# Optimization experiments

Measured on AMD Instinct MI355X. Metric: run time of the kernel, lower is better.

## Reference

```python
import jax, jax.numpy as jnp
import numpy as np

N = 100000   # n_nodes
E = 500000   # n_edges
EH = 256     # e_hidden
RH = 128     # r_hidden
R = 1000     # n_relations (rel.max()+1, pinned in setup)


def _seg_softmax(logits, seg, num_segments):
    # numerically-stable softmax grouped by segment id
    m = jax.ops.segment_max(logits, seg, num_segments=num_segments)
    ex = jnp.exp(logits - m[seg])
    s = jax.ops.segment_sum(ex, seg, num_segments=num_segments)
    return ex / s[seg]


def setup_inputs() -> dict:
    key = jax.random.key(0)
    ks = jax.random.split(key, 14)
    s_e = 1.0 / np.sqrt(EH)
    s_r = 1.0 / np.sqrt(RH)
    x_e = jax.random.normal(ks[0], (N, EH), dtype=jnp.float32)
    edge_index = jax.random.randint(ks[1], (2, E), 0, N, dtype=jnp.int32)
    rel = jax.random.randint(ks[2], (E,), 0, R, dtype=jnp.int32).at[0].set(R - 1)
    rel_all = jax.random.randint(ks[3], (E,), 0, R, dtype=jnp.int32)
    return {
        "x_e": x_e,
        "edge_index": edge_index,
        "rel": rel,
        "rel_all": rel_all,
        "w_h": jax.random.normal(ks[4], (EH, RH), dtype=jnp.float32) * s_e,
        "w_t": jax.random.normal(ks[5], (EH, RH), dtype=jnp.float32) * s_e,
        "a_h1": jax.random.normal(ks[6], (RH,), dtype=jnp.float32) * s_r,
        "a_h2": jax.random.normal(ks[7], (RH,), dtype=jnp.float32) * s_r,
        "a_t1": jax.random.normal(ks[8], (RH,), dtype=jnp.float32) * s_r,
        "a_t2": jax.random.normal(ks[9], (RH,), dtype=jnp.float32) * s_r,
        "r_h_w": jax.random.normal(ks[10], (RH, RH), dtype=jnp.float32) * s_r,
        "r_h_b": jax.random.normal(ks[11], (RH,), dtype=jnp.float32) * s_r,
        "r_t_w": jax.random.normal(ks[12], (RH, RH), dtype=jnp.float32) * s_r,
        "r_t_b": jax.random.normal(ks[13], (RH,), dtype=jnp.float32) * s_r,
    }


def reference(x_e, edge_index, rel, rel_all, w_h, w_t, a_h1, a_h2, a_t1, a_t2,
              r_h_w, r_h_b, r_t_w, r_t_b):
    h_idx, t_idx = edge_index[0], edge_index[1]
    x_r_h = x_e @ w_h          # [N, RH]
    x_r_t = x_e @ w_t          # [N, RH]
    # per-node attention scalars, gathered per edge
    e1 = (x_r_h @ a_h1)[h_idx] + (x_r_t @ a_h2)[t_idx]   # [E]
    e2 = (x_r_h @ a_t1)[h_idx] + (x_r_t @ a_t2)[t_idx]   # [E]
    alpha_h = _seg_softmax(jax.nn.leaky_relu(e1, 0.01), rel, R)
    alpha_t = _seg_softmax(jax.nn.leaky_relu(e2, 0.01), rel, R)
    # sparse.mm(adj, M) == segment-sum over edges of alpha[e] * M[node[e]] into row rel[e]
    msg_h = x_r_h @ r_h_w + r_h_b + x_r_h                 # [N, RH]
    msg_t = x_r_t @ r_t_w + r_t_b + x_r_t                 # [N, RH]
    out_h = jax.ops.segment_sum(alpha_h[:, None] * msg_h[h_idx], rel, num_segments=R)
    out_t = jax.ops.segment_sum(alpha_t[:, None] * msg_t[t_idx], rel, num_segments=R)
    return out_h + out_t                                   # [R, RH]
```

## Files before the change

### kernel.cpp

```cpp
#include <hip/hip_runtime.h>
#include <hip/hip_bf16.h>
#include <math.h>


#define EHD 256
#define RHD 128
#define RMAX 1024
#define HBLK 128
#define SCHUNK 2048
#define SEGMAX 4096

typedef __attribute__((ext_vector_type(8))) short short8;
typedef __attribute__((ext_vector_type(4))) float f32x4;

__device__ __forceinline__ short f2bf(float x) {
    __hip_bfloat16 b = __float2bfloat16(x);
    return *reinterpret_cast<short*>(&b);
}
__device__ __forceinline__ float bfu(unsigned int u) {
    return __uint_as_float(u << 16);
}
__device__ __forceinline__ float leaky(float x) { return x > 0.f ? x : 0.01f * x; }
__device__ __forceinline__ int xswz(int row, int col) {
    return col ^ ((row & 7) << 3);
}

__global__ __launch_bounds__(256) void k_prep2(const float* __restrict__ wh,
                                               const float* __restrict__ wt,
                                               short* __restrict__ whT,
                                               short* __restrict__ wtT)
{
    const float* src = blockIdx.z ? wt : wh;
    short* dst = blockIdx.z ? wtT : whT;
    __shared__ float t[32][33];
    const int k0 = blockIdx.x * 32, n0 = blockIdx.y * 32;
    const int tr = threadIdx.x >> 3, tc = (threadIdx.x & 7) << 2;
    float4 v = *reinterpret_cast<const float4*>(src + (size_t)(k0 + tr) * RHD + n0 + tc);
    t[tr][tc + 0] = v.x; t[tr][tc + 1] = v.y;
    t[tr][tc + 2] = v.z; t[tr][tc + 3] = v.w;
    __syncthreads();
    short* o = dst + (size_t)(n0 + tr) * EHD + k0 + tc;
    o[0] = f2bf(t[tc + 0][tr]); o[1] = f2bf(t[tc + 1][tr]);
    o[2] = f2bf(t[tc + 2][tr]); o[3] = f2bf(t[tc + 3][tr]);
}

__global__ __launch_bounds__(256, 4) void k_fused(
    const float* __restrict__ xe,
    const short* __restrict__ whT, const short* __restrict__ wtT,
    const float* __restrict__ ah1, const float* __restrict__ ah2,
    const float* __restrict__ at1, const float* __restrict__ at2,
    float2* __restrict__ sA, float2* __restrict__ sB,
    short* __restrict__ xrh, short* __restrict__ xrt, int N,
    const int* __restrict__ rel, int* __restrict__ counts, int R, int E)
{
    __shared__ __align__(16) union {
        short Bs[2][2][128][32];
        short Xs[2][64][128];
        int   Hs[RMAX];
    } u;

    const int tid = threadIdx.x;
    const int w = tid >> 6, l = tid & 63;
    const int ln = l & 15, lk = l >> 4;
    const int m0 = blockIdx.x * 64;
    const int orow = (w << 4) + (lk << 2);

    f32x4 acch[8], acct[8];
#pragma unroll
    for (int c = 0; c < 8; c++) {
        acch[c] = (f32x4){0.f, 0.f, 0.f, 0.f};
        acct[c] = (f32x4){0.f, 0.f, 0.f, 0.f};
    }

    const int arow = m0 + (w << 4) + ln;
    const int aclamp = min(arow, N - 1);
    const float* abase = xe + (size_t)aclamp * EHD + (lk << 3);
    short* BsFlat = &u.Bs[0][0][0][0];

    const int Rl = l >> 2, kc = l & 3;

    auto stage = [&](int buf, int kt) {
#pragma unroll
        for (int i = 0; i < 4; i++) {
            const int j = (w << 2) + i;
            const int Rr = (j << 4) + Rl;
            const int mat = Rr >> 7, row = Rr & 127;
            const short* g = (mat ? wtT : whT) + (size_t)row * EHD + kt + (kc << 3);
            __builtin_amdgcn_global_load_lds(
                (const __attribute__((address_space(1))) void*)g,
                (__attribute__((address_space(3))) void*)(BsFlat + (buf << 13) + (j << 9)),
                16, 0, 0);
        }
    };

    float4 a0 = *reinterpret_cast<const float4*>(abase);
    float4 a1 = *reinterpret_cast<const float4*>(abase + 4);
    stage(0, 0);

#pragma unroll
    for (int s = 0; s < 8; s++) {
        const int kt = s << 5;
        __syncthreads();
        if (s < 7) stage((s + 1) & 1, kt + 32);
        short8 af;
        af[0] = f2bf(a0.x); af[1] = f2bf(a0.y); af[2] = f2bf(a0.z); af[3] = f2bf(a0.w);
        af[4] = f2bf(a1.x); af[5] = f2bf(a1.y); af[6] = f2bf(a1.z); af[7] = f2bf(a1.w);
        if (s < 7) {
            a0 = *reinterpret_cast<const float4*>(abase + kt + 32);
            a1 = *reinterpret_cast<const float4*>(abase + kt + 36);
        }
        const int b = s & 1;
#pragma unroll
        for (int c = 0; c < 8; c++) {
            short8 bh = *reinterpret_cast<const short8*>(&u.Bs[b][0][(c << 4) + ln][lk << 3]);
            short8 bt = *reinterpret_cast<const short8*>(&u.Bs[b][1][(c << 4) + ln][lk << 3]);
            acch[c] = __builtin_amdgcn_mfma_f32_16x16x32_bf16(af, bh, acch[c], 0, 0, 0);
            acct[c] = __builtin_amdgcn_mfma_f32_16x16x32_bf16(af, bt, acct[c], 0, 0, 0);
        }
    }
    __syncthreads();

    float p1[4] = {0,0,0,0}, p2[4] = {0,0,0,0}, p3[4] = {0,0,0,0}, p4[4] = {0,0,0,0};
#pragma unroll
    for (int c = 0; c < 8; c++) {
        const int col = (c << 4) + ln;
        const float wa1 = ah1[col], wa2 = ah2[col], wa3 = at1[col], wa4 = at2[col];
#pragma unroll
        for (int r = 0; r < 4; r++) {
            const float vh = acch[c][r], vt = acct[c][r];
            p1[r] = fmaf(vh, wa1, p1[r]);
            p3[r] = fmaf(vh, wa3, p3[r]);
            p2[r] = fmaf(vt, wa2, p2[r]);
            p4[r] = fmaf(vt, wa4, p4[r]);
            const int row = orow + r;
            const int cs = xswz(row, col);
            u.Xs[0][row][cs] = f2bf(vh);
            u.Xs[1][row][cs] = f2bf(vt);
        }
    }
#pragma unroll
    for (int off = 1; off < 16; off <<= 1) {
#pragma unroll
        for (int r = 0; r < 4; r++) {
            p1[r] += __shfl_xor(p1[r], off);
            p2[r] += __shfl_xor(p2[r], off);
            p3[r] += __shfl_xor(p3[r], off);
            p4[r] += __shfl_xor(p4[r], off);
        }
    }
    if (ln == 0) {
#pragma unroll
        for (int r = 0; r < 4; r++) {
            const int grow = m0 + orow + r;
            if (grow < N) {
                sA[grow] = make_float2(p1[r], p3[r]);
                sB[grow] = make_float2(p2[r], p4[r]);
            }
        }
    }
    __syncthreads();
#pragma unroll
    for (int it = 0; it < 8; it++) {
        const int idx = tid + (it << 8);
        const int mat = idx >> 10;
        const int rem = idx & 1023;
        const int row = rem >> 4;
        const int ch  = rem & 15;
        const int grow = m0 + row;
        if (grow < N) {
            const int cs = (ch << 3) ^ ((row & 7) << 3);
            short8 v = *reinterpret_cast<const short8*>(&u.Xs[mat][row][cs]);
            short* dst = (mat ? xrt : xrh) + (size_t)grow * RHD + (ch << 3);
            *reinterpret_cast<short8*>(dst) = v;
        }
    }

    if (blockIdx.x < HBLK) {
        __syncthreads();
        for (int i = tid; i < R; i += 256) u.Hs[i] = 0;
        __syncthreads();
        for (int e = blockIdx.x * 256 + tid; e < E; e += HBLK * 256)
            atomicAdd(&u.Hs[rel[e]], 1);
        __syncthreads();
        for (int i = tid; i < R; i += 256) {
            int v = u.Hs[i];
            if (v) atomicAdd(&counts[i], v);
        }
    }
}

__global__ __launch_bounds__(1024) void k_scan(
    const int* __restrict__ counts, int* __restrict__ starts,
    int* __restrict__ cursor, int R, int E)
{
    __shared__ int buf[2][1024];
    int t = threadIdx.x;
    int v = (t < R) ? counts[t] : 0;
    buf[0][t] = v;
    int cur = 0;
    for (int off = 1; off < 1024; off <<= 1) {
        __syncthreads();
        int x = buf[cur][t];
        if (t >= off) x += buf[cur][t - off];
        buf[cur ^ 1][t] = x;
        cur ^= 1;
    }
    __syncthreads();
    int incl = buf[cur][t];
    if (t < R) { starts[t] = incl - v; cursor[t] = incl - v; }
    if (t == 0) starts[R] = E;
}

__global__ __launch_bounds__(256) void k_scatter(
    const int* __restrict__ rel, int* __restrict__ cursor,
    const int* __restrict__ eh, const int* __restrict__ et,
    const float2* __restrict__ sA, const float2* __restrict__ sB,
    int2* __restrict__ rec1, int2* __restrict__ rec2, int R, int E)
{
    __shared__ int lcnt[RMAX];
    __shared__ int lbase[RMAX];
    const int tid = threadIdx.x;
    const int base = blockIdx.x * SCHUNK;
    const int nE = min(SCHUNK, E - base);
    for (int i = tid; i < R; i += 256) lcnt[i] = 0;
    __syncthreads();
    for (int i = tid; i < nE; i += 256) atomicAdd(&lcnt[rel[base + i]], 1);
    __syncthreads();
    for (int r = tid; r < R; r += 256) {
        int c = lcnt[r];
        lbase[r] = c ? atomicAdd(&cursor[r], c) : 0;
        lcnt[r] = 0;
    }
    __syncthreads();
    for (int i = tid; i < nE; i += 256) {
        const int e = base + i;
        const int r = rel[e];
        const int off = atomicAdd(&lcnt[r], 1);
        const int pos = lbase[r] + off;
        const int h = eh[e], t = et[e];
        const float2 va = sA[h];
        const float2 vb = sB[t];
        const float x1 = __expf(leaky(va.x + vb.x));
        const float x2 = __expf(leaky(va.y + vb.y));
        rec1[pos] = make_int2(h, __float_as_int(x1));
        rec2[pos] = make_int2(t, __float_as_int(x2));
    }
}

__global__ __launch_bounds__(512) void k_rel(
    const int* __restrict__ starts,
    const int2* __restrict__ rec1, const int2* __restrict__ rec2,
    const short* __restrict__ xrh, const short* __restrict__ xrt,
    float* __restrict__ y, int R)
{
    const int r = blockIdx.x;
    const int side = blockIdx.y;
    const int start = starts[r], end = starts[r + 1];
    const int len = end - start;
    if (len <= 0) return;
    const int tid = threadIdx.x;
    const int2* __restrict__ rc = (side ? rec2 : rec1) + start;
    const unsigned short* __restrict__ mb =
        reinterpret_cast<const unsigned short*>(side ? xrt : xrh);

    __shared__ float red[8];
    __shared__ int   lnode[SEGMAX];
    __shared__ float lal[SEGMAX];
    __shared__ float part[8][128];

    const int slot = tid >> 6;
    const int jj = tid & 63;
    float a0 = 0.f, a1 = 0.f;

    if (len <= SEGMAX) {
        float sum = 0.f;
        for (int i = tid; i < len; i += 512) {
            int2 v = rc[i];
            lnode[i] = v.x;
            float x = __int_as_float(v.y);
            lal[i] = x;
            sum += x;
        }
#pragma unroll
        for (int off = 32; off > 0; off >>= 1) sum += __shfl_xor(sum, off);
        if ((tid & 63) == 0) red[slot] = sum;
        __syncthreads();
        sum = ((red[0] + red[1]) + (red[2] + red[3]))
            + ((red[4] + red[5]) + (red[6] + red[7]));
        const float inv = 1.f / sum;

        int q = slot;
        for (; q + 24 < len; q += 32) {
            const float w0 = lal[q] * inv;       const int n0 = lnode[q];
            const float w1 = lal[q + 8] * inv;   const int n1 = lnode[q + 8];
            const float w2 = lal[q + 16] * inv;  const int n2 = lnode[q + 16];
            const float w3 = lal[q + 24] * inv;  const int n3 = lnode[q + 24];
            const unsigned int v0 =
                *reinterpret_cast<const unsigned int*>(mb + (size_t)n0 * RHD + (jj << 1));
            const unsigned int v1 =
                *reinterpret_cast<const unsigned int*>(mb + (size_t)n1 * RHD + (jj << 1));
            const unsigned int v2 =
                *reinterpret_cast<const unsigned int*>(mb + (size_t)n2 * RHD + (jj << 1));
            const unsigned int v3 =
                *reinterpret_cast<const unsigned int*>(mb + (size_t)n3 * RHD + (jj << 1));
            a0 = fmaf(w0, bfu(v0 & 0xffffu), a0);
            a1 = fmaf(w0, bfu(v0 >> 16), a1);
            a0 = fmaf(w1, bfu(v1 & 0xffffu), a0);
            a1 = fmaf(w1, bfu(v1 >> 16), a1);
            a0 = fmaf(w2, bfu(v2 & 0xffffu), a0);
            a1 = fmaf(w2, bfu(v2 >> 16), a1);
            a0 = fmaf(w3, bfu(v3 & 0xffffu), a0);
            a1 = fmaf(w3, bfu(v3 >> 16), a1);
        }
        for (; q < len; q += 8) {
            const float w0 = lal[q] * inv;
            const int   n0 = lnode[q];
            const unsigned int v0 =
                *reinterpret_cast<const unsigned int*>(mb + (size_t)n0 * RHD + (jj << 1));
            a0 = fmaf(w0, bfu(v0 & 0xffffu), a0);
            a1 = fmaf(w0, bfu(v0 >> 16), a1);
        }
    } else {
        float sum = 0.f;
        for (int i = tid; i < len; i += 512) sum += __int_as_float(rc[i].y);
#pragma unroll
        for (int off = 32; off > 0; off >>= 1) sum += __shfl_xor(sum, off);
        if ((tid & 63) == 0) red[slot] = sum;
        __syncthreads();
        sum = ((red[0] + red[1]) + (red[2] + red[3]))
            + ((red[4] + red[5]) + (red[6] + red[7]));
        const float inv = 1.f / sum;

        for (int c0 = 0; c0 < len; c0 += 512) {
            __syncthreads();
            int i = c0 + tid;
            if (i < len) {
                int2 v = rc[i];
                lal[tid] = __int_as_float(v.y) * inv;
                lnode[tid] = v.x;
            }
            __syncthreads();
            const int nc = min(512, len - c0);
            for (int q = slot; q < nc; q += 8) {
                const float wq = lal[q];
                const int n = lnode[q];
                const unsigned int v =
                    *reinterpret_cast<const unsigned int*>(mb + (size_t)n * RHD + (jj << 1));
                a0 = fmaf(wq, bfu(v & 0xffffu), a0);
                a1 = fmaf(wq, bfu(v >> 16), a1);
            }
        }
    }

    part[slot][(jj << 1) + 0] = a0;
    part[slot][(jj << 1) + 1] = a1;
    __syncthreads();
    if (tid < 128) {
        float v = ((part[0][tid] + part[1][tid]) + (part[2][tid] + part[3][tid]))
                + ((part[4][tid] + part[5][tid]) + (part[6][tid] + part[7][tid]));
        y[((size_t)side * R + r) * RHD + tid] = v;
    }
}

__global__ __launch_bounds__(128) void k_out(
    const float* __restrict__ y,
    const float* __restrict__ rhw, const float* __restrict__ rtw,
    const float* __restrict__ rhb, const float* __restrict__ rtb,
    const int* __restrict__ starts,
    float* __restrict__ out, int R)
{
    const int r = blockIdx.x;
    const int j = threadIdx.x;
    __shared__ float ph[RHD], pt[RHD];
    ph[j] = y[(size_t)r * RHD + j];
    pt[j] = y[((size_t)R + r) * RHD + j];
    __syncthreads();
    float acc = ph[j] + pt[j];
    if (starts[r + 1] > starts[r]) acc += rhb[j] + rtb[j];
    float a = 0.f;
#pragma unroll 8
    for (int k = 0; k < RHD; k++) {
        a = fmaf(ph[k], rhw[k * RHD + j], a);
        a = fmaf(pt[k], rtw[k * RHD + j], a);
    }
    out[(size_t)r * RHD + j] = acc + a;
}

extern "C" void kernel_launch(void* const* d_in, const int* in_sizes, int n_in,
                              void* d_out, int out_size, void* d_ws, size_t ws_size,
                              hipStream_t stream)
{
    const float* xe  = (const float*)d_in[0];
    const int*  eidx = (const int*)d_in[1];
    const int*  rel  = (const int*)d_in[2];
    const float* wh  = (const float*)d_in[4];
    const float* wt  = (const float*)d_in[5];
    const float* ah1 = (const float*)d_in[6];
    const float* ah2 = (const float*)d_in[7];
    const float* at1 = (const float*)d_in[8];
    const float* at2 = (const float*)d_in[9];
    const float* rhw = (const float*)d_in[10];
    const float* rhb = (const float*)d_in[11];
    const float* rtw = (const float*)d_in[12];
    const float* rtb = (const float*)d_in[13];
    float* out = (float*)d_out;

    const int N = in_sizes[0] / EHD;
    const int E = in_sizes[2];
    const int R = out_size / RHD;
    const int* eh = eidx;
    const int* et = eidx + E;

    char* ws = (char*)d_ws;
    size_t off = 0;
    auto alloc = [&](size_t bytes) -> void* {
        void* p = ws + off;
        off = (off + bytes + 255) & ~(size_t)255;
        return p;
    };
    short* xrh   = (short*)alloc((size_t)N * RHD * sizeof(short));
    short* xrt   = (short*)alloc((size_t)N * RHD * sizeof(short));
    short* whT   = (short*)alloc((size_t)RHD * EHD * sizeof(short));
    short* wtT   = (short*)alloc((size_t)RHD * EHD * sizeof(short));
    float* y     = (float*)alloc((size_t)2 * R * RHD * sizeof(float));
    float2* sA   = (float2*)alloc((size_t)N * sizeof(float2));
    float2* sB   = (float2*)alloc((size_t)N * sizeof(float2));
    int* counts  = (int*)alloc((size_t)R * sizeof(int));
    int* starts  = (int*)alloc((size_t)(R + 1) * sizeof(int));
    int* cursor  = (int*)alloc((size_t)R * sizeof(int));
    int2* rec1   = (int2*)alloc((size_t)E * sizeof(int2));
    int2* rec2   = (int2*)alloc((size_t)E * sizeof(int2));
    (void)ws_size; (void)n_in;

    hipMemsetAsync(counts, 0, (size_t)R * sizeof(int), stream);
    hipMemsetAsync(y, 0, (size_t)2 * R * RHD * sizeof(float), stream);

    k_prep2<<<dim3(EHD / 32, RHD / 32, 2), 256, 0, stream>>>(wh, wt, whT, wtT);

    k_fused<<<(N + 63) / 64, 256, 0, stream>>>(
        xe, whT, wtT, ah1, ah2, at1, at2,
        sA, sB, xrh, xrt, N, rel, counts, R, E);

    k_scan<<<1, 1024, 0, stream>>>(counts, starts, cursor, R, E);
    k_scatter<<<(E + SCHUNK - 1) / SCHUNK, 256, 0, stream>>>(
        rel, cursor, eh, et, sA, sB, rec1, rec2, R, E);
    k_rel<<<dim3(R, 2), 512, 0, stream>>>(starts, rec1, rec2, xrh, xrt, y, R);
    k_out<<<R, 128, 0, stream>>>(y, rhw, rtw, rhb, rtb, starts, out, R);
}
```

Measured before the change: 122.4 us.

## Fold prefix scan into fused kernel via last-block pattern; merge edge records

Removes the separate single-block scan kernel launch by having the last block of the fused GEMM kernel, detected with a completion counter and thread fences, compute the exclusive prefix over relation counts. It also merges the two per-edge int2 record arrays into one int4 array, so the scatter issues a single 16-byte store per edge. The cost is an extra memset and an atomic per block. k_rel now reads 16 bytes per edge where it needs only 8, which doubles its record traffic.

```diff
diff --git a/kernel.cpp b/kernel.cpp
--- a/kernel.cpp
+++ b/kernel.cpp
@@ -51,13 +51,17 @@
     const float* __restrict__ at1, const float* __restrict__ at2,
     float2* __restrict__ sA, float2* __restrict__ sB,
     short* __restrict__ xrh, short* __restrict__ xrt, int N,
-    const int* __restrict__ rel, int* __restrict__ counts, int R, int E)
+    const int* __restrict__ rel, int* __restrict__ counts,
+    int* __restrict__ starts, int* __restrict__ cursor,
+    int* __restrict__ donecnt, int R, int E)
 {
     __shared__ __align__(16) union {
         short Bs[2][2][128][32];
         short Xs[2][64][128];
         int   Hs[RMAX];
+        int   Sc[2][RMAX];
     } u;
+    __shared__ int lastflag;
 
     const int tid = threadIdx.x;
     const int w = tid >> 6, l = tid & 63;
@@ -187,35 +191,43 @@
             if (v) atomicAdd(&counts[i], v);
         }
     }
-}
-
-__global__ __launch_bounds__(1024) void k_scan(
-    const int* __restrict__ counts, int* __restrict__ starts,
-    int* __restrict__ cursor, int R, int E)
-{
-    __shared__ int buf[2][1024];
-    int t = threadIdx.x;
-    int v = (t < R) ? counts[t] : 0;
-    buf[0][t] = v;
-    int cur = 0;
-    for (int off = 1; off < 1024; off <<= 1) {
-        __syncthreads();
-        int x = buf[cur][t];
-        if (t >= off) x += buf[cur][t - off];
-        buf[cur ^ 1][t] = x;
-        cur ^= 1;
-    }
-    __syncthreads();
-    int incl = buf[cur][t];
-    if (t < R) { starts[t] = incl - v; cursor[t] = incl - v; }
-    if (t == 0) starts[R] = E;
+
+    __threadfence();
+    if (tid == 0) {
+        int prev = atomicAdd(donecnt, 1);
+        lastflag = (prev == (int)gridDim.x - 1);
+    }
+    __syncthreads();
+    if (lastflag) {
+        __threadfence();
+        __syncthreads();
+        for (int i = tid; i < RMAX; i += 256)
+            u.Sc[0][i] = (i < R) ? counts[i] : 0;
+        __syncthreads();
+        int cur = 0;
+        for (int off = 1; off < RMAX; off <<= 1) {
+            for (int i = tid; i < RMAX; i += 256) {
+                int x = u.Sc[cur][i];
+                if (i >= off) x += u.Sc[cur][i - off];
+                u.Sc[cur ^ 1][i] = x;
+            }
+            __syncthreads();
+            cur ^= 1;
+        }
+        for (int i = tid; i < R; i += 256) {
+            const int st = u.Sc[cur][i] - counts[i];
+            starts[i] = st;
+            cursor[i] = st;
+        }
+        if (tid == 0) starts[R] = E;
+    }
 }
 
 __global__ __launch_bounds__(256) void k_scatter(
     const int* __restrict__ rel, int* __restrict__ cursor,
     const int* __restrict__ eh, const int* __restrict__ et,
     const float2* __restrict__ sA, const float2* __restrict__ sB,
-    int2* __restrict__ rec1, int2* __restrict__ rec2, int R, int E)
+    int4* __restrict__ rec, int R, int E)
 {
     __shared__ int lcnt[RMAX];
     __shared__ int lbase[RMAX];
@@ -242,14 +254,13 @@
         const float2 vb = sB[t];
         const float x1 = __expf(leaky(va.x + vb.x));
         const float x2 = __expf(leaky(va.y + vb.y));
-        rec1[pos] = make_int2(h, __float_as_int(x1));
-        rec2[pos] = make_int2(t, __float_as_int(x2));
+        rec[pos] = make_int4(h, __float_as_int(x1), t, __float_as_int(x2));
     }
 }
 
 __global__ __launch_bounds__(512) void k_rel(
     const int* __restrict__ starts,
-    const int2* __restrict__ rec1, const int2* __restrict__ rec2,
+    const int4* __restrict__ rec,
     const short* __restrict__ xrh, const short* __restrict__ xrt,
     float* __restrict__ y, int R)
 {
@@ -259,7 +270,7 @@
     const int len = end - start;
     if (len <= 0) return;
     const int tid = threadIdx.x;
-    const int2* __restrict__ rc = (side ? rec2 : rec1) + start;
+    const int4* __restrict__ rc = rec + start;
     const unsigned short* __restrict__ mb =
         reinterpret_cast<const unsigned short*>(side ? xrt : xrh);
 
@@ -275,9 +286,10 @@
     if (len <= SEGMAX) {
         float sum = 0.f;
         for (int i = tid; i < len; i += 512) {
-            int2 v = rc[i];
-            lnode[i] = v.x;
-            float x = __int_as_float(v.y);
+            int4 v = rc[i];
+            const int node = side ? v.z : v.x;
+            const float x = __int_as_float(side ? v.w : v.y);
+            lnode[i] = node;
             lal[i] = x;
             sum += x;
         }
@@ -322,7 +334,8 @@
         }
     } else {
         float sum = 0.f;
-        for (int i = tid; i < len; i += 512) sum += __int_as_float(rc[i].y);
+        for (int i = tid; i < len; i += 512)
+            sum += __int_as_float(side ? rc[i].w : rc[i].y);
 #pragma unroll
         for (int off = 32; off > 0; off >>= 1) sum += __shfl_xor(sum, off);
         if ((tid & 63) == 0) red[slot] = sum;
@@ -335,9 +348,9 @@
             __syncthreads();
             int i = c0 + tid;
             if (i < len) {
-                int2 v = rc[i];
-                lal[tid] = __int_as_float(v.y) * inv;
-                lnode[tid] = v.x;
+                int4 v = rc[i];
+                lnode[tid] = side ? v.z : v.x;
+                lal[tid] = __int_as_float(side ? v.w : v.y) * inv;
             }
             __syncthreads();
             const int nc = min(512, len - c0);
@@ -428,22 +441,22 @@
     int* counts  = (int*)alloc((size_t)R * sizeof(int));
     int* starts  = (int*)alloc((size_t)(R + 1) * sizeof(int));
     int* cursor  = (int*)alloc((size_t)R * sizeof(int));
-    int2* rec1   = (int2*)alloc((size_t)E * sizeof(int2));
-    int2* rec2   = (int2*)alloc((size_t)E * sizeof(int2));
+    int* donecnt = (int*)alloc(sizeof(int));
+    int4* rec    = (int4*)alloc((size_t)E * sizeof(int4));
     (void)ws_size; (void)n_in;
 
     hipMemsetAsync(counts, 0, (size_t)R * sizeof(int), stream);
+    hipMemsetAsync(donecnt, 0, sizeof(int), stream);
     hipMemsetAsync(y, 0, (size_t)2 * R * RHD * sizeof(float), stream);
 
     k_prep2<<<dim3(EHD / 32, RHD / 32, 2), 256, 0, stream>>>(wh, wt, whT, wtT);
 
     k_fused<<<(N + 63) / 64, 256, 0, stream>>>(
         xe, whT, wtT, ah1, ah2, at1, at2,
-        sA, sB, xrh, xrt, N, rel, counts, R, E);
-
-    k_scan<<<1, 1024, 0, stream>>>(counts, starts, cursor, R, E);
+        sA, sB, xrh, xrt, N, rel, counts, starts, cursor, donecnt, R, E);
+
     k_scatter<<<(E + SCHUNK - 1) / SCHUNK, 256, 0, stream>>>(
-        rel, cursor, eh, et, sA, sB, rec1, rec2, R, E);
-    k_rel<<<dim3(R, 2), 512, 0, stream>>>(starts, rec1, rec2, xrh, xrt, y, R);
+        rel, cursor, eh, et, sA, sB, rec, R, E);
+    k_rel<<<dim3(R, 2), 512, 0, stream>>>(starts, rec, xrh, xrt, y, R);
     k_out<<<R, 128, 0, stream>>>(y, rhw, rtw, rhb, rtb, starts, out, R);
 }
```

Result: slower. 311.0 us (+154.1%).
